# Optimization experiments

Hardware: AMD Instinct MI355X
Metric: run time of the kernel (lower is better)

## Reference

```python
import jax, jax.numpy as jnp
import numpy as np

NEG_INF = -100000.0
NUM_HEADS = 16


def setup_inputs() -> dict:
    key = jax.random.key(0)
    ks = jax.random.split(key, 6)
    B, S, D = 2, 2048, 1024
    scale = 0.02
    return {
        "x": jax.random.normal(ks[0], (B, S, D), dtype=jnp.float32),
        "Wq": jax.random.normal(ks[1], (D, D), dtype=jnp.float32) * scale,
        "Wk": jax.random.normal(ks[2], (D, D), dtype=jnp.float32) * scale,
        "Wv": jax.random.normal(ks[3], (D, D), dtype=jnp.float32) * scale,
        "Wo": jax.random.normal(ks[4], (D, D), dtype=jnp.float32) * scale,
        "bo": jnp.zeros((D,), dtype=jnp.float32),
    }


def reference(x, Wq, Wk, Wv, Wo, bo):
    B, S, D = x.shape
    H = NUM_HEADS
    hd = D // H
    # QKV projections (no bias), split heads: [B, H, S, hd]
    q = (x @ Wq).reshape(B, S, H, hd).transpose(0, 2, 1, 3)
    k = (x @ Wk).reshape(B, S, H, hd).transpose(0, 2, 1, 3)
    v = (x @ Wv).reshape(B, S, H, hd).transpose(0, 2, 1, 3)
    # scaled dot-product scores [B, H, S, S]
    scores = jnp.einsum("bhqd,bhkd->bhqk", q, k) / jnp.sqrt(jnp.float32(hd))
    # causal mask: True above diagonal -> filled with NEG_INF (not -inf, faithful to source)
    causal = jnp.triu(jnp.ones((S, S), dtype=bool), k=1)
    scores = jnp.where(causal, NEG_INF, scores)
    attn = jax.nn.softmax(scores, axis=-1)  # dropout p=0.0 -> identity
    ctx = jnp.einsum("bhqk,bhkd->bhqd", attn, v)
    ctx = ctx.transpose(0, 2, 1, 3).reshape(B, S, D)
    out = ctx @ Wo + bo
    return out, attn
```

## Files before the change

### kernel.cpp

```cpp
#include <hip/hip_runtime.h>

#define S_   2048
#define D_   1024
#define H_   16
#define HD_  64
#define B_   2
#define BH_  32
#define M_   4096
#define SCALE 0.125f

typedef short s8v  __attribute__((ext_vector_type(8)));
typedef float f4v  __attribute__((ext_vector_type(4)));
typedef unsigned short us4v __attribute__((ext_vector_type(4)));
typedef unsigned short us8v __attribute__((ext_vector_type(8)));

__device__ inline unsigned short f2b(float f) {
    unsigned u = __builtin_bit_cast(unsigned, f);
    return (unsigned short)((u + 0x7fffu + ((u >> 16) & 1u)) >> 16);
}

__global__ __launch_bounds__(256) void conv_x(const float* __restrict__ in,
                                              unsigned short* __restrict__ out) {
    int i = blockIdx.x * 256 + threadIdx.x;
    float4 v = ((const float4*)in)[i];
    us4v o = { f2b(v.x), f2b(v.y), f2b(v.z), f2b(v.w) };
    *(us4v*)&out[(size_t)i * 4] = o;
}

__global__ __launch_bounds__(256) void convT(
    const float* __restrict__ W0, const float* __restrict__ W1,
    const float* __restrict__ W2, const float* __restrict__ W3,
    unsigned short* __restrict__ WtAll) {
    const int z = blockIdx.z;
    const float* W = (z == 0) ? W0 : (z == 1) ? W1 : (z == 2) ? W2 : W3;
    unsigned short* Wt = WtAll + (size_t)z * D_ * D_;
    __shared__ unsigned short Tb[64][65];
    const int t = threadIdx.x;
    const int r0 = blockIdx.y * 64, c0 = blockIdx.x * 64;
    #pragma unroll
    for (int j = 0; j < 4; ++j) {
        int v = j * 256 + t; int r = v >> 4, c4 = (v & 15) * 4;
        float4 wv = *(const float4*)&W[(size_t)(r0 + r) * D_ + c0 + c4];
        Tb[r][c4 + 0] = f2b(wv.x); Tb[r][c4 + 1] = f2b(wv.y);
        Tb[r][c4 + 2] = f2b(wv.z); Tb[r][c4 + 3] = f2b(wv.w);
    }
    __syncthreads();
    #pragma unroll
    for (int j = 0; j < 2; ++j) {
        int v = j * 256 + t; int c = v >> 3, r8 = (v & 7) * 8;
        us8v o;
        #pragma unroll
        for (int i = 0; i < 8; ++i) o[i] = Tb[r8 + i][c];
        *(us8v*)&Wt[(size_t)(c0 + c) * D_ + r0 + r8] = o;
    }
}

__global__ __launch_bounds__(256) void qkv_mfma(
    const unsigned short* __restrict__ xb, const unsigned short* __restrict__ WtAll,
    unsigned short* __restrict__ Qb, unsigned short* __restrict__ Kb,
    unsigned short* __restrict__ Vt) {
    const int z = blockIdx.z;
    const unsigned short* Wp = WtAll + (size_t)z * D_ * D_;
    const int bm = blockIdx.y, bn = blockIdx.x;
    const int t = threadIdx.x;
    const int w = t >> 6, lane = t & 63;
    const int lg = lane >> 4, lid = lane & 15;
    const int wm = w >> 1, wn = w & 1;

    __shared__ unsigned short As[128][72];
    __shared__ unsigned short Bs[128][72];

    const f4v z4 = {0.f, 0.f, 0.f, 0.f};
    f4v acc[4][4];
    #pragma unroll
    for (int mf = 0; mf < 4; ++mf)
        #pragma unroll
        for (int nf = 0; nf < 4; ++nf) acc[mf][nf] = z4;

    for (int bk = 0; bk < 16; ++bk) {
        #pragma unroll
        for (int j = 0; j < 4; ++j) {
            int v = j * 256 + t; int r = v >> 3, c8 = (v & 7) * 8;
            *(us8v*)&As[r][c8] = *(const us8v*)&xb[(size_t)(bm * 128 + r) * D_ + bk * 64 + c8];
            *(us8v*)&Bs[r][c8] = *(const us8v*)&Wp[(size_t)(bn * 128 + r) * D_ + bk * 64 + c8];
        }
        __syncthreads();
        #pragma unroll
        for (int kk = 0; kk < 2; ++kk) {
            s8v af[4], bf[4];
            #pragma unroll
            for (int mf = 0; mf < 4; ++mf)
                af[mf] = *(const s8v*)&As[wm * 64 + mf * 16 + lid][kk * 32 + lg * 8];
            #pragma unroll
            for (int nf = 0; nf < 4; ++nf)
                bf[nf] = *(const s8v*)&Bs[wn * 64 + nf * 16 + lid][kk * 32 + lg * 8];
            #pragma unroll
            for (int mf = 0; mf < 4; ++mf)
                #pragma unroll
                for (int nf = 0; nf < 4; ++nf)
                    acc[mf][nf] = __builtin_amdgcn_mfma_f32_16x16x32_bf16(
                        af[mf], bf[nf], acc[mf][nf], 0, 0, 0);
        }
        __syncthreads();
    }

    const int rbase = lg * 4;
    if (z == 2) {
        #pragma unroll
        for (int mf = 0; mf < 4; ++mf) {
            const int m0 = bm * 128 + wm * 64 + mf * 16 + rbase;
            const int b = m0 >> 11, s0 = m0 & (S_ - 1);
            #pragma unroll
            for (int nf = 0; nf < 4; ++nf) {
                const int n = bn * 128 + wn * 64 + nf * 16 + lid;
                const int h = n >> 6, d = n & 63;
                us4v o;
                #pragma unroll
                for (int r = 0; r < 4; ++r) o[r] = f2b(acc[mf][nf][r]);
                *(us4v*)&Vt[((size_t)((b * H_ + h) * HD_ + d)) * S_ + s0] = o;
            }
        }
    } else {
        unsigned short* O = (z == 0) ? Qb : Kb;
        #pragma unroll
        for (int mf = 0; mf < 4; ++mf) {
            #pragma unroll
            for (int r = 0; r < 4; ++r) {
                const int m = bm * 128 + wm * 64 + mf * 16 + rbase + r;
                const int b = m >> 11, s = m & (S_ - 1);
                #pragma unroll
                for (int nf = 0; nf < 4; ++nf) {
                    const int n = bn * 128 + wn * 64 + nf * 16 + lid;
                    const int h = n >> 6, d = n & 63;
                    O[((size_t)((b * H_ + h) * S_ + s)) * HD_ + d] = f2b(acc[mf][nf][r]);
                }
            }
        }
    }
}

__global__ __launch_bounds__(256) void attn_fused(
    const unsigned short* __restrict__ Qb, const unsigned short* __restrict__ Kb,
    const unsigned short* __restrict__ Vt, float* __restrict__ attn,
    unsigned short* __restrict__ ctxb) {
    const int bh = blockIdx.x;
    const int qt = 31 - (int)blockIdx.y;
    const int t = threadIdx.x, w = t >> 6, lane = t & 63;
    const int lg = lane >> 4, lid = lane & 15;

    __shared__ unsigned short Pt[4][16][72];
    __shared__ float Pf[64][68];

    const unsigned short* Qp = Qb + ((size_t)bh * S_ + qt * 64 + w * 16 + lid) * HD_;
    const s8v qf0 = *(const s8v*)&Qp[lg * 8];
    const s8v qf1 = *(const s8v*)&Qp[32 + lg * 8];

    const unsigned short* Kbase = Kb + (size_t)bh * S_ * HD_;
    const unsigned short* Vbase = Vt + (size_t)bh * HD_ * S_;
    float* abase = attn + (size_t)bh * S_ * S_;

    const f4v z4 = {0.f, 0.f, 0.f, 0.f};
    const int nkt = qt + 1;
    const int qrow_base = qt * 64 + w * 16 + lg * 4;

    float sp[4] = {0.f, 0.f, 0.f, 0.f};
    for (int kt = 0; kt < nkt; ++kt) {
        f4v sacc[4];
        #pragma unroll
        for (int nf = 0; nf < 4; ++nf) sacc[nf] = z4;
        #pragma unroll
        for (int nf = 0; nf < 4; ++nf) {
            const unsigned short* Kr = Kbase + ((size_t)(kt * 64 + nf * 16 + lid)) * HD_;
            s8v b0 = *(const s8v*)&Kr[lg * 8];
            s8v b1 = *(const s8v*)&Kr[32 + lg * 8];
            sacc[nf] = __builtin_amdgcn_mfma_f32_16x16x32_bf16(qf0, b0, sacc[nf], 0, 0, 0);
            sacc[nf] = __builtin_amdgcn_mfma_f32_16x16x32_bf16(qf1, b1, sacc[nf], 0, 0, 0);
        }
        const bool diag = (kt == qt);
        #pragma unroll
        for (int r = 0; r < 4; ++r) {
            const int qrow = qrow_base + r;
            #pragma unroll
            for (int nf = 0; nf < 4; ++nf) {
                float e = __expf(sacc[nf][r] * SCALE);
                if (diag && (kt * 64 + nf * 16 + lid) > qrow) e = 0.f;
                sp[r] += e;
            }
        }
    }
    float invs[4];
    #pragma unroll
    for (int r = 0; r < 4; ++r) {
        float s = sp[r];
        #pragma unroll
        for (int mk = 8; mk; mk >>= 1) s += __shfl_xor(s, mk);
        invs[r] = 1.0f / s;
    }

    f4v cacc[4];
    #pragma unroll
    for (int nf = 0; nf < 4; ++nf) cacc[nf] = z4;

    for (int kt = 0; kt < nkt; ++kt) {
        f4v sacc[4];
        #pragma unroll
        for (int nf = 0; nf < 4; ++nf) sacc[nf] = z4;
        #pragma unroll
        for (int nf = 0; nf < 4; ++nf) {
            const unsigned short* Kr = Kbase + ((size_t)(kt * 64 + nf * 16 + lid)) * HD_;
            s8v b0 = *(const s8v*)&Kr[lg * 8];
            s8v b1 = *(const s8v*)&Kr[32 + lg * 8];
            sacc[nf] = __builtin_amdgcn_mfma_f32_16x16x32_bf16(qf0, b0, sacc[nf], 0, 0, 0);
            sacc[nf] = __builtin_amdgcn_mfma_f32_16x16x32_bf16(qf1, b1, sacc[nf], 0, 0, 0);
        }
        const bool diag = (kt == qt);
        #pragma unroll
        for (int r = 0; r < 4; ++r) {
            const int qrow = qrow_base + r;
            #pragma unroll
            for (int nf = 0; nf < 4; ++nf) {
                float p = __expf(sacc[nf][r] * SCALE) * invs[r];
                if (diag && (kt * 64 + nf * 16 + lid) > qrow) p = 0.f;
                Pf[w * 16 + lg * 4 + r][nf * 16 + lid] = p;
                Pt[w][lg * 4 + r][nf * 16 + lid] = f2b(p);
            }
        }
        __syncthreads();
        {
            const int row = t >> 2, c0 = t & 3;
            float* dst = &abase[(size_t)(qt * 64 + row) * S_ + kt * 64];
            #pragma unroll
            for (int i = 0; i < 4; ++i) {
                const int c4 = c0 + i * 4;
                *(float4*)&dst[c4 * 4] = *(const float4*)&Pf[row][c4 * 4];
            }
        }
        #pragma unroll
        for (int ks = 0; ks < 2; ++ks) {
            s8v pa = *(const s8v*)&Pt[w][lid][ks * 32 + lg * 8];
            #pragma unroll
            for (int nf = 0; nf < 4; ++nf) {
                s8v vb = *(const s8v*)&Vbase[((size_t)(nf * 16 + lid)) * S_ +
                                             kt * 64 + ks * 32 + lg * 8];
                cacc[nf] = __builtin_amdgcn_mfma_f32_16x16x32_bf16(pa, vb, cacc[nf], 0, 0, 0);
            }
        }
        __syncthreads();
    }

    const int b = bh >> 4, h = bh & (H_ - 1);
    #pragma unroll
    for (int nf = 0; nf < 4; ++nf) {
        #pragma unroll
        for (int r = 0; r < 4; ++r) {
            const int s = qt * 64 + w * 16 + lg * 4 + r;
            ctxb[((size_t)(b * S_ + s)) * D_ + h * HD_ + nf * 16 + lid] = f2b(cacc[nf][r]);
        }
    }

    const int c0 = (qt + 1) * 64;
    const float4 zz = make_float4(0.f, 0.f, 0.f, 0.f);
    const int row = t >> 2;
    for (int c = c0 + (t & 3) * 4; c < S_; c += 16)
        *(float4*)&abase[(size_t)(qt * 64 + row) * S_ + c] = zz;
}

__global__ __launch_bounds__(256) void out_mfma(
    const unsigned short* __restrict__ ctxb, const unsigned short* __restrict__ Wot,
    const float* __restrict__ bo, float* __restrict__ out) {
    const int bm = blockIdx.y, bn = blockIdx.x;
    const int t = threadIdx.x;
    const int w = t >> 6, lane = t & 63;
    const int lg = lane >> 4, lid = lane & 15;
    const int wm = w >> 1, wn = w & 1;

    __shared__ unsigned short As[128][72];
    __shared__ unsigned short Bs[128][72];

    const f4v z4 = {0.f, 0.f, 0.f, 0.f};
    f4v acc[4][4];
    #pragma unroll
    for (int mf = 0; mf < 4; ++mf)
        #pragma unroll
        for (int nf = 0; nf < 4; ++nf) acc[mf][nf] = z4;

    for (int bk = 0; bk < 16; ++bk) {
        #pragma unroll
        for (int j = 0; j < 4; ++j) {
            int v = j * 256 + t; int r = v >> 3, c8 = (v & 7) * 8;
            *(us8v*)&As[r][c8] = *(const us8v*)&ctxb[(size_t)(bm * 128 + r) * D_ + bk * 64 + c8];
            *(us8v*)&Bs[r][c8] = *(const us8v*)&Wot[(size_t)(bn * 128 + r) * D_ + bk * 64 + c8];
        }
        __syncthreads();
        #pragma unroll
        for (int kk = 0; kk < 2; ++kk) {
            s8v af[4], bf[4];
            #pragma unroll
            for (int mf = 0; mf < 4; ++mf)
                af[mf] = *(const s8v*)&As[wm * 64 + mf * 16 + lid][kk * 32 + lg * 8];
            #pragma unroll
            for (int nf = 0; nf < 4; ++nf)
                bf[nf] = *(const s8v*)&Bs[wn * 64 + nf * 16 + lid][kk * 32 + lg * 8];
            #pragma unroll
            for (int mf = 0; mf < 4; ++mf)
                #pragma unroll
                for (int nf = 0; nf < 4; ++nf)
                    acc[mf][nf] = __builtin_amdgcn_mfma_f32_16x16x32_bf16(
                        af[mf], bf[nf], acc[mf][nf], 0, 0, 0);
        }
        __syncthreads();
    }

    #pragma unroll
    for (int mf = 0; mf < 4; ++mf) {
        #pragma unroll
        for (int r = 0; r < 4; ++r) {
            const int m = bm * 128 + wm * 64 + mf * 16 + lg * 4 + r;
            #pragma unroll
            for (int nf = 0; nf < 4; ++nf) {
                const int n = bn * 128 + wn * 64 + nf * 16 + lid;
                out[(size_t)m * D_ + n] = acc[mf][nf][r] + bo[n];
            }
        }
    }
}

extern "C" void kernel_launch(void* const* d_in, const int* in_sizes, int n_in,
                              void* d_out, int out_size, void* d_ws, size_t ws_size,
                              hipStream_t stream) {
    const float* x  = (const float*)d_in[0];
    const float* Wq = (const float*)d_in[1];
    const float* Wk = (const float*)d_in[2];
    const float* Wv = (const float*)d_in[3];
    const float* Wo = (const float*)d_in[4];
    const float* bo = (const float*)d_in[5];

    float* out  = (float*)d_out;
    float* attn = out + (size_t)M_ * D_;

    unsigned short* ws   = (unsigned short*)d_ws;
    unsigned short* xb   = ws;
    unsigned short* Wt   = xb + (size_t)M_ * D_;
    unsigned short* Qb   = Wt + (size_t)4 * D_ * D_;
    unsigned short* Kb   = Qb + (size_t)M_ * D_;
    unsigned short* Vt   = Kb + (size_t)M_ * D_;
    unsigned short* ctxb = Vt + (size_t)M_ * D_;

    conv_x<<<dim3((M_ * D_) / 4 / 256), 256, 0, stream>>>(x, xb);
    convT<<<dim3(16, 16, 4), 256, 0, stream>>>(Wq, Wk, Wv, Wo, Wt);
    qkv_mfma<<<dim3(8, 32, 3), 256, 0, stream>>>(xb, Wt, Qb, Kb, Vt);
    attn_fused<<<dim3(32, 32), 256, 0, stream>>>(Qb, Kb, Vt, attn, ctxb);
    out_mfma<<<dim3(8, 32), 256, 0, stream>>>(ctxb, Wt + (size_t)3 * D_ * D_, bo, out);
}
```

Baseline: 843.1 us.

## Split fused attention into per-tile denominator, probability-write and PV kernels

The single attention kernel, one block per query tile, is replaced by a pipeline. It zeroes the row sums, then computes them per (query tile, key tile) block over the causal triangle using atomics. Separate kernels write the upper zero tail and the normalized probabilities per triangle tile. A PV kernel then rereads the fp32 probabilities from global memory, converts them to bf16 and multiplies by V. The aim is to remove the load imbalance of long diagonal rows and expose far more blocks. The cost is extra launches, atomics and a full reread of the causal half of the attention matrix.

```diff
diff --git a/kernel.cpp b/kernel.cpp
--- a/kernel.cpp
+++ b/kernel.cpp
@@ -8,6 +8,7 @@
 #define BH_  32
 #define M_   4096
 #define SCALE 0.125f
+#define NTRI 528
 
 typedef short s8v  __attribute__((ext_vector_type(8)));
 typedef float f4v  __attribute__((ext_vector_type(4)));
@@ -17,6 +18,13 @@
 __device__ inline unsigned short f2b(float f) {
     unsigned u = __builtin_bit_cast(unsigned, f);
     return (unsigned short)((u + 0x7fffu + ((u >> 16) & 1u)) >> 16);
+}
+
+__device__ inline void tri_map(int L, int& qt, int& kt) {
+    int q = (int)((sqrtf(8.0f * (float)L + 1.0f) - 1.0f) * 0.5f);
+    while ((q + 1) * (q + 2) / 2 <= L) ++q;
+    while (q * (q + 1) / 2 > L) --q;
+    qt = q; kt = L - q * (q + 1) / 2;
 }
 
 __global__ __launch_bounds__(256) void conv_x(const float* __restrict__ in,
@@ -139,113 +147,148 @@
     }
 }
 
-__global__ __launch_bounds__(256) void attn_fused(
+__global__ __launch_bounds__(256) void zero_rowsum(float* __restrict__ p) {
+    int i = blockIdx.x * 256 + threadIdx.x;
+    ((float4*)p)[i] = make_float4(0.f, 0.f, 0.f, 0.f);
+}
+
+__global__ __launch_bounds__(256) void denom_k(
     const unsigned short* __restrict__ Qb, const unsigned short* __restrict__ Kb,
-    const unsigned short* __restrict__ Vt, float* __restrict__ attn,
+    float* __restrict__ rowsum) {
+    const int bh = blockIdx.x;
+    int qt, kt; tri_map(blockIdx.y, qt, kt);
+    const int t = threadIdx.x, w = t >> 6, lane = t & 63;
+    const int lg = lane >> 4, lid = lane & 15;
+
+    const unsigned short* Qp = Qb + ((size_t)bh * S_ + qt * 64 + w * 16 + lid) * HD_;
+    const s8v qf0 = *(const s8v*)&Qp[lg * 8];
+    const s8v qf1 = *(const s8v*)&Qp[32 + lg * 8];
+    const unsigned short* Kbase = Kb + (size_t)bh * S_ * HD_;
+
+    const f4v z4 = {0.f, 0.f, 0.f, 0.f};
+    f4v sacc[4];
+    #pragma unroll
+    for (int nf = 0; nf < 4; ++nf) sacc[nf] = z4;
+    #pragma unroll
+    for (int nf = 0; nf < 4; ++nf) {
+        const unsigned short* Kr = Kbase + ((size_t)(kt * 64 + nf * 16 + lid)) * HD_;
+        s8v b0 = *(const s8v*)&Kr[lg * 8];
+        s8v b1 = *(const s8v*)&Kr[32 + lg * 8];
+        sacc[nf] = __builtin_amdgcn_mfma_f32_16x16x32_bf16(qf0, b0, sacc[nf], 0, 0, 0);
+        sacc[nf] = __builtin_amdgcn_mfma_f32_16x16x32_bf16(qf1, b1, sacc[nf], 0, 0, 0);
+    }
+    const bool diag = (kt == qt);
+    #pragma unroll
+    for (int r = 0; r < 4; ++r) {
+        const int qrow = qt * 64 + w * 16 + lg * 4 + r;
+        float s = 0.f;
+        #pragma unroll
+        for (int nf = 0; nf < 4; ++nf) {
+            float e = __expf(sacc[nf][r] * SCALE);
+            if (diag && (kt * 64 + nf * 16 + lid) > qrow) e = 0.f;
+            s += e;
+        }
+        #pragma unroll
+        for (int mk = 8; mk; mk >>= 1) s += __shfl_xor(s, mk);
+        if (lid == 0) atomicAdd(&rowsum[(size_t)bh * S_ + qrow], s);
+    }
+}
+
+__global__ __launch_bounds__(256) void ztail(float* __restrict__ attn) {
+    const int bh = blockIdx.x, qt = blockIdx.y;
+    float* abase = attn + (size_t)bh * S_ * S_;
+    const int t = threadIdx.x;
+    const int row = t >> 2;
+    const float4 zz = make_float4(0.f, 0.f, 0.f, 0.f);
+    for (int c = (qt + 1) * 64 + (t & 3) * 4; c < S_; c += 16)
+        *(float4*)&attn[(size_t)bh * S_ * S_ + (size_t)(qt * 64 + row) * S_ + c] = zz;
+    (void)abase;
+}
+
+__global__ __launch_bounds__(256) void pwrite(
+    const unsigned short* __restrict__ Qb, const unsigned short* __restrict__ Kb,
+    const float* __restrict__ rowsum, float* __restrict__ attn) {
+    const int bh = blockIdx.x;
+    int qt, kt; tri_map(blockIdx.y, qt, kt);
+    const int t = threadIdx.x, w = t >> 6, lane = t & 63;
+    const int lg = lane >> 4, lid = lane & 15;
+
+    __shared__ float Pf[64][68];
+
+    const unsigned short* Qp = Qb + ((size_t)bh * S_ + qt * 64 + w * 16 + lid) * HD_;
+    const s8v qf0 = *(const s8v*)&Qp[lg * 8];
+    const s8v qf1 = *(const s8v*)&Qp[32 + lg * 8];
+    const unsigned short* Kbase = Kb + (size_t)bh * S_ * HD_;
+
+    const f4v z4 = {0.f, 0.f, 0.f, 0.f};
+    f4v sacc[4];
+    #pragma unroll
+    for (int nf = 0; nf < 4; ++nf) sacc[nf] = z4;
+    #pragma unroll
+    for (int nf = 0; nf < 4; ++nf) {
+        const unsigned short* Kr = Kbase + ((size_t)(kt * 64 + nf * 16 + lid)) * HD_;
+        s8v b0 = *(const s8v*)&Kr[lg * 8];
+        s8v b1 = *(const s8v*)&Kr[32 + lg * 8];
+        sacc[nf] = __builtin_amdgcn_mfma_f32_16x16x32_bf16(qf0, b0, sacc[nf], 0, 0, 0);
+        sacc[nf] = __builtin_amdgcn_mfma_f32_16x16x32_bf16(qf1, b1, sacc[nf], 0, 0, 0);
+    }
+    const bool diag = (kt == qt);
+    #pragma unroll
+    for (int r = 0; r < 4; ++r) {
+        const int qrow = qt * 64 + w * 16 + lg * 4 + r;
+        const float inv = 1.0f / rowsum[(size_t)bh * S_ + qrow];
+        #pragma unroll
+        for (int nf = 0; nf < 4; ++nf) {
+            float p = __expf(sacc[nf][r] * SCALE) * inv;
+            if (diag && (kt * 64 + nf * 16 + lid) > qrow) p = 0.f;
+            Pf[w * 16 + lg * 4 + r][nf * 16 + lid] = p;
+        }
+    }
+    __syncthreads();
+    {
+        const int row = t >> 2, c0 = t & 3;
+        float* dst = &attn[(size_t)bh * S_ * S_ + (size_t)(qt * 64 + row) * S_ + kt * 64];
+        #pragma unroll
+        for (int i = 0; i < 4; ++i) {
+            const int c4 = c0 + i * 4;
+            *(float4*)&dst[c4 * 4] = *(const float4*)&Pf[row][c4 * 4];
+        }
+    }
+}
+
+__global__ __launch_bounds__(256) void pv_k(
+    const float* __restrict__ attn, const unsigned short* __restrict__ Vt,
     unsigned short* __restrict__ ctxb) {
     const int bh = blockIdx.x;
     const int qt = 31 - (int)blockIdx.y;
     const int t = threadIdx.x, w = t >> 6, lane = t & 63;
     const int lg = lane >> 4, lid = lane & 15;
 
-    __shared__ unsigned short Pt[4][16][72];
-    __shared__ float Pf[64][68];
-
-    const unsigned short* Qp = Qb + ((size_t)bh * S_ + qt * 64 + w * 16 + lid) * HD_;
-    const s8v qf0 = *(const s8v*)&Qp[lg * 8];
-    const s8v qf1 = *(const s8v*)&Qp[32 + lg * 8];
-
-    const unsigned short* Kbase = Kb + (size_t)bh * S_ * HD_;
+    const float* Pr = attn + (size_t)bh * S_ * S_ + (size_t)(qt * 64 + w * 16 + lid) * S_;
     const unsigned short* Vbase = Vt + (size_t)bh * HD_ * S_;
-    float* abase = attn + (size_t)bh * S_ * S_;
-
-    const f4v z4 = {0.f, 0.f, 0.f, 0.f};
-    const int nkt = qt + 1;
-    const int qrow_base = qt * 64 + w * 16 + lg * 4;
-
-    float sp[4] = {0.f, 0.f, 0.f, 0.f};
-    for (int kt = 0; kt < nkt; ++kt) {
-        f4v sacc[4];
-        #pragma unroll
-        for (int nf = 0; nf < 4; ++nf) sacc[nf] = z4;
+
+    const f4v z4 = {0.f, 0.f, 0.f, 0.f};
+    f4v cacc[4];
+    #pragma unroll
+    for (int nf = 0; nf < 4; ++nf) cacc[nf] = z4;
+
+    for (int kt = 0; kt <= qt; ++kt) {
+        float4 a0 = *(const float4*)&Pr[kt * 64 + lg * 8];
+        float4 a1 = *(const float4*)&Pr[kt * 64 + lg * 8 + 4];
+        float4 a2 = *(const float4*)&Pr[kt * 64 + 32 + lg * 8];
+        float4 a3 = *(const float4*)&Pr[kt * 64 + 32 + lg * 8 + 4];
+        s8v pa0 = { (short)f2b(a0.x), (short)f2b(a0.y), (short)f2b(a0.z), (short)f2b(a0.w),
+                    (short)f2b(a1.x), (short)f2b(a1.y), (short)f2b(a1.z), (short)f2b(a1.w) };
+        s8v pa1 = { (short)f2b(a2.x), (short)f2b(a2.y), (short)f2b(a2.z), (short)f2b(a2.w),
+                    (short)f2b(a3.x), (short)f2b(a3.y), (short)f2b(a3.z), (short)f2b(a3.w) };
         #pragma unroll
         for (int nf = 0; nf < 4; ++nf) {
-            const unsigned short* Kr = Kbase + ((size_t)(kt * 64 + nf * 16 + lid)) * HD_;
-            s8v b0 = *(const s8v*)&Kr[lg * 8];
-            s8v b1 = *(const s8v*)&Kr[32 + lg * 8];
-            sacc[nf] = __builtin_amdgcn_mfma_f32_16x16x32_bf16(qf0, b0, sacc[nf], 0, 0, 0);
-            sacc[nf] = __builtin_amdgcn_mfma_f32_16x16x32_bf16(qf1, b1, sacc[nf], 0, 0, 0);
-        }
-        const bool diag = (kt == qt);
-        #pragma unroll
-        for (int r = 0; r < 4; ++r) {
-            const int qrow = qrow_base + r;
-            #pragma unroll
-            for (int nf = 0; nf < 4; ++nf) {
-                float e = __expf(sacc[nf][r] * SCALE);
-                if (diag && (kt * 64 + nf * 16 + lid) > qrow) e = 0.f;
-                sp[r] += e;
-            }
-        }
-    }
-    float invs[4];
-    #pragma unroll
-    for (int r = 0; r < 4; ++r) {
-        float s = sp[r];
-        #pragma unroll
-        for (int mk = 8; mk; mk >>= 1) s += __shfl_xor(s, mk);
-        invs[r] = 1.0f / s;
-    }
-
-    f4v cacc[4];
-    #pragma unroll
-    for (int nf = 0; nf < 4; ++nf) cacc[nf] = z4;
-
-    for (int kt = 0; kt < nkt; ++kt) {
-        f4v sacc[4];
-        #pragma unroll
-        for (int nf = 0; nf < 4; ++nf) sacc[nf] = z4;
-        #pragma unroll
-        for (int nf = 0; nf < 4; ++nf) {
-            const unsigned short* Kr = Kbase + ((size_t)(kt * 64 + nf * 16 + lid)) * HD_;
-            s8v b0 = *(const s8v*)&Kr[lg * 8];
-            s8v b1 = *(const s8v*)&Kr[32 + lg * 8];
-            sacc[nf] = __builtin_amdgcn_mfma_f32_16x16x32_bf16(qf0, b0, sacc[nf], 0, 0, 0);
-            sacc[nf] = __builtin_amdgcn_mfma_f32_16x16x32_bf16(qf1, b1, sacc[nf], 0, 0, 0);
-        }
-        const bool diag = (kt == qt);
-        #pragma unroll
-        for (int r = 0; r < 4; ++r) {
-            const int qrow = qrow_base + r;
-            #pragma unroll
-            for (int nf = 0; nf < 4; ++nf) {
-                float p = __expf(sacc[nf][r] * SCALE) * invs[r];
-                if (diag && (kt * 64 + nf * 16 + lid) > qrow) p = 0.f;
-                Pf[w * 16 + lg * 4 + r][nf * 16 + lid] = p;
-                Pt[w][lg * 4 + r][nf * 16 + lid] = f2b(p);
-            }
-        }
-        __syncthreads();
-        {
-            const int row = t >> 2, c0 = t & 3;
-            float* dst = &abase[(size_t)(qt * 64 + row) * S_ + kt * 64];
-            #pragma unroll
-            for (int i = 0; i < 4; ++i) {
-                const int c4 = c0 + i * 4;
-                *(float4*)&dst[c4 * 4] = *(const float4*)&Pf[row][c4 * 4];
-            }
-        }
-        #pragma unroll
-        for (int ks = 0; ks < 2; ++ks) {
-            s8v pa = *(const s8v*)&Pt[w][lid][ks * 32 + lg * 8];
-            #pragma unroll
-            for (int nf = 0; nf < 4; ++nf) {
-                s8v vb = *(const s8v*)&Vbase[((size_t)(nf * 16 + lid)) * S_ +
-                                             kt * 64 + ks * 32 + lg * 8];
-                cacc[nf] = __builtin_amdgcn_mfma_f32_16x16x32_bf16(pa, vb, cacc[nf], 0, 0, 0);
-            }
-        }
-        __syncthreads();
+            const unsigned short* Vr = &Vbase[((size_t)(nf * 16 + lid)) * S_ + kt * 64];
+            s8v vb0 = *(const s8v*)&Vr[lg * 8];
+            s8v vb1 = *(const s8v*)&Vr[32 + lg * 8];
+            cacc[nf] = __builtin_amdgcn_mfma_f32_16x16x32_bf16(pa0, vb0, cacc[nf], 0, 0, 0);
+            cacc[nf] = __builtin_amdgcn_mfma_f32_16x16x32_bf16(pa1, vb1, cacc[nf], 0, 0, 0);
+        }
     }
 
     const int b = bh >> 4, h = bh & (H_ - 1);
@@ -257,12 +300,6 @@
             ctxb[((size_t)(b * S_ + s)) * D_ + h * HD_ + nf * 16 + lid] = f2b(cacc[nf][r]);
         }
     }
-
-    const int c0 = (qt + 1) * 64;
-    const float4 zz = make_float4(0.f, 0.f, 0.f, 0.f);
-    const int row = t >> 2;
-    for (int c = c0 + (t & 3) * 4; c < S_; c += 16)
-        *(float4*)&abase[(size_t)(qt * 64 + row) * S_ + c] = zz;
 }
 
 __global__ __launch_bounds__(256) void out_mfma(
@@ -345,10 +382,15 @@
     unsigned short* Kb   = Qb + (size_t)M_ * D_;
     unsigned short* Vt   = Kb + (size_t)M_ * D_;
     unsigned short* ctxb = Vt + (size_t)M_ * D_;
+    float* rowsum        = (float*)(ctxb + (size_t)M_ * D_);
 
     conv_x<<<dim3((M_ * D_) / 4 / 256), 256, 0, stream>>>(x, xb);
     convT<<<dim3(16, 16, 4), 256, 0, stream>>>(Wq, Wk, Wv, Wo, Wt);
     qkv_mfma<<<dim3(8, 32, 3), 256, 0, stream>>>(xb, Wt, Qb, Kb, Vt);
-    attn_fused<<<dim3(32, 32), 256, 0, stream>>>(Qb, Kb, Vt, attn, ctxb);
+    zero_rowsum<<<dim3((BH_ * S_) / 4 / 256), 256, 0, stream>>>(rowsum);
+    denom_k<<<dim3(BH_, NTRI), 256, 0, stream>>>(Qb, Kb, rowsum);
+    ztail<<<dim3(BH_, 32), 256, 0, stream>>>(attn);
+    pwrite<<<dim3(BH_, NTRI), 256, 0, stream>>>(Qb, Kb, rowsum, attn);
+    pv_k<<<dim3(BH_, 32), 256, 0, stream>>>(attn, Vt, ctxb);
     out_mfma<<<dim3(8, 32), 256, 0, stream>>>(ctxb, Wt + (size_t)3 * D_ * D_, bo, out);
 }
```

Result: slower. 1.004 ms (+19.1%).
